# Kernel optimization log

Hardware: AMD Instinct MI355X
Metric: run time of the kernel (lower is better)

## Reference

```python
import jax, jax.numpy as jnp
import numpy as np

N = 96   # collocation points per axis
H = 64   # MLP hidden width (features[:-1])
R = 32   # CP rank (r * out_dim with out_dim=1)


def setup_inputs() -> dict:
    key = jax.random.key(0)
    ks = jax.random.split(key, 7)

    def glorot(k, shape, fan_in, fan_out):
        s = np.sqrt(2.0 / (fan_in + fan_out)).astype(np.float32)
        return jax.random.normal(k, shape, jnp.float32) * s

    return {
        "t": jax.random.uniform(ks[0], (N, 1), jnp.float32),
        "x": jax.random.uniform(ks[1], (N, 1), jnp.float32),
        "y": jax.random.uniform(ks[2], (N, 1), jnp.float32),
        "z": jax.random.uniform(ks[3], (N, 1), jnp.float32),
        "W1": glorot(ks[4], (4, 1, H), 1, H),
        "b1": jnp.zeros((4, H), jnp.float32),
        "W2": glorot(ks[5], (4, H, H), H, H),
        "b2": jnp.zeros((4, H), jnp.float32),
        "W3": glorot(ks[6], (4, H, R), H, R),
        "b3": jnp.zeros((4, R), jnp.float32),
    }


def reference(t, x, y, z, W1, b1, W2, b2, W3, b3):
    coords = (t, x, y, z)
    outs = []
    for i in range(4):  # fixed small loop over the 4 axes (distinct params)
        h = jnp.tanh(coords[i] @ W1[i] + b1[i])   # [N, H]
        h = jnp.tanh(h @ W2[i] + b2[i])           # [N, H]
        o = h @ W3[i] + b3[i]                     # [N, R]
        outs.append(o.T)                          # [R, N]
    ft, fx, fy, fz = outs
    tx = jnp.einsum('ft,fx->ftx', ft, fx)         # [R, Nt, Nx]
    txy = jnp.einsum('ftx,fy->ftxy', tx, fy)      # [R, Nt, Nx, Ny]
    pred = jnp.einsum('ftxy,fz->txyz', txy, fz)   # [Nt, Nx, Ny, Nz]
    return pred
```

## Files before the change

kernel.cpp:

```cpp
#include <hip/hip_runtime.h>

#define NPTS 96
#define HID  64
#define RANK 32

typedef float f2 __attribute__((ext_vector_type(2)));
typedef float f4 __attribute__((ext_vector_type(4)));

__global__ __launch_bounds__(64) void spinn_mlp(
    const float* __restrict__ t, const float* __restrict__ x,
    const float* __restrict__ y, const float* __restrict__ z,
    const float* __restrict__ W1, const float* __restrict__ b1,
    const float* __restrict__ W2, const float* __restrict__ b2,
    const float* __restrict__ W3, const float* __restrict__ b3,
    float* __restrict__ ws)
{
    const int n    = blockIdx.x;
    const int axis = blockIdx.y;
    const int j    = threadIdx.x;

    const float* coords[4] = { t, x, y, z };
    const float c = coords[axis][n];

    __shared__ float h1[HID];
    __shared__ float h2[HID];

    h1[j] = tanhf(fmaf(c, W1[axis * HID + j], b1[axis * HID + j]));
    __syncthreads();

    float a = b2[axis * HID + j];
    #pragma unroll
    for (int k = 0; k < HID; ++k)
        a = fmaf(h1[k], W2[(axis * HID + k) * HID + j], a);
    h2[j] = tanhf(a);
    __syncthreads();

    if (j < RANK) {
        float o = b3[axis * RANK + j];
        #pragma unroll
        for (int k = 0; k < HID; ++k)
            o = fmaf(h2[k], W3[(axis * HID + k) * RANK + j], o);
        ws[axis * RANK * NPTS + j * NPTS + n]             = o;
        ws[4 * RANK * NPTS + (axis * NPTS + n) * RANK + j] = o;
    }
}

__global__ __launch_bounds__(192) void spinn_outer(
    const float* __restrict__ ws, float* __restrict__ out)
{
    const float* plain = ws;
    const float* trans = ws + 4 * RANK * NPTS;

    const int tt  = blockIdx.x;
    const int yb  = blockIdx.y;
    const int xh  = blockIdx.z;
    const int tid = threadIdx.x;
    const int yq  = tid / 24;
    const int z4  = tid % 24;
    const int yy  = yb * 8 + yq;
    const int z0  = z4 * 4;

    const float* ftT = trans + (0 * NPTS + tt) * RANK;
    const float* fyT = trans + (2 * NPTS + yy) * RANK;
    const float* fzP = plain + 3 * RANK * NPTS;

    f2 q0[RANK], q1[RANK];
    #pragma unroll
    for (int f = 0; f < RANK; ++f) {
        const float g = ftT[f] * fyT[f];
        const float* fzf = fzP + f * NPTS + z0;
        f2 a = { fzf[0], fzf[1] };
        f2 b = { fzf[2], fzf[3] };
        q0[f] = a * g;
        q1[f] = b * g;
    }

    const float* fxT = trans + 1 * NPTS * RANK;
    const int x0 = xh * 48;
    const size_t outb = (size_t)tt * NPTS * NPTS * NPTS + (size_t)yy * NPTS + z0;

    for (int xs = 0; xs < 48; ++xs) {
        const int xx = x0 + xs;
        const float* __restrict__ fx = fxT + xx * RANK;
        f2 acc0 = { 0.f, 0.f }, acc1 = { 0.f, 0.f };
        #pragma unroll
        for (int f = 0; f < RANK; ++f) {
            const float s = fx[f];
            const f2 s2 = { s, s };
            acc0 = __builtin_elementwise_fma(s2, q0[f], acc0);
            acc1 = __builtin_elementwise_fma(s2, q1[f], acc1);
        }
        f4 res = { acc0.x, acc0.y, acc1.x, acc1.y };
        f4* dst = (f4*)(out + outb + (size_t)xx * NPTS * NPTS);
        __builtin_nontemporal_store(res, dst);
    }
}

extern "C" void kernel_launch(void* const* d_in, const int* in_sizes, int n_in,
                              void* d_out, int out_size, void* d_ws, size_t ws_size,
                              hipStream_t stream)
{
    const float* t  = (const float*)d_in[0];
    const float* x  = (const float*)d_in[1];
    const float* y  = (const float*)d_in[2];
    const float* z  = (const float*)d_in[3];
    const float* W1 = (const float*)d_in[4];
    const float* b1 = (const float*)d_in[5];
    const float* W2 = (const float*)d_in[6];
    const float* b2 = (const float*)d_in[7];
    const float* W3 = (const float*)d_in[8];
    const float* b3 = (const float*)d_in[9];

    float* ws  = (float*)d_ws;
    float* out = (float*)d_out;

    spinn_mlp<<<dim3(NPTS, 4), 64, 0, stream>>>(t, x, y, z, W1, b1, W2, b2, W3, b3, ws);

    spinn_outer<<<dim3(NPTS, 12, 2), 192, 0, stream>>>(ws, out);
}
```

Measured before the change: 90.01 us.

## Pack rank pairs into packed FMAs and defer output stores one iteration

Rewrites the outer-product inner loop to pair adjacent rank components, so each packed FMA consumes two rank terms at once. fx values are loaded as float4 vectors. Each output store is deferred to the next iteration behind a sched barrier, letting the store overlap the next row's loads and math. The change adds inline asm v_pk_fma_f32, extra accumulators and a final horizontal reduction, which changes summation order slightly and raises register pressure.

```diff
diff --git a/kernel.cpp b/kernel.cpp
--- a/kernel.cpp
+++ b/kernel.cpp
@@ -6,6 +6,8 @@
 
 typedef float f2 __attribute__((ext_vector_type(2)));
 typedef float f4 __attribute__((ext_vector_type(4)));
+
+#define TRANS_OFF (4 * RANK * NPTS)
 
 __global__ __launch_bounds__(64) void spinn_mlp(
     const float* __restrict__ t, const float* __restrict__ x,
@@ -40,17 +42,14 @@
         #pragma unroll
         for (int k = 0; k < HID; ++k)
             o = fmaf(h2[k], W3[(axis * HID + k) * RANK + j], o);
-        ws[axis * RANK * NPTS + j * NPTS + n]             = o;
-        ws[4 * RANK * NPTS + (axis * NPTS + n) * RANK + j] = o;
+        ws[axis * RANK * NPTS + j * NPTS + n]        = o;
+        ws[TRANS_OFF + (axis * NPTS + n) * RANK + j] = o;
     }
 }
 
 __global__ __launch_bounds__(192) void spinn_outer(
     const float* __restrict__ ws, float* __restrict__ out)
 {
-    const float* plain = ws;
-    const float* trans = ws + 4 * RANK * NPTS;
-
     const int tt  = blockIdx.x;
     const int yb  = blockIdx.y;
     const int xh  = blockIdx.z;
@@ -60,40 +59,80 @@
     const int yy  = yb * 8 + yq;
     const int z0  = z4 * 4;
 
-    const float* ftT = trans + (0 * NPTS + tt) * RANK;
-    const float* fyT = trans + (2 * NPTS + yy) * RANK;
-    const float* fzP = plain + 3 * RANK * NPTS;
+    const float* ftT = ws + TRANS_OFF + (0 * NPTS + tt) * RANK;
+    const float* fyT = ws + TRANS_OFF + (2 * NPTS + yy) * RANK;
+    const float* fzP = ws + 3 * RANK * NPTS;
 
-    f2 q0[RANK], q1[RANK];
+    f2 q2[16][4];
     #pragma unroll
-    for (int f = 0; f < RANK; ++f) {
-        const float g = ftT[f] * fyT[f];
-        const float* fzf = fzP + f * NPTS + z0;
-        f2 a = { fzf[0], fzf[1] };
-        f2 b = { fzf[2], fzf[3] };
-        q0[f] = a * g;
-        q1[f] = b * g;
+    for (int k = 0; k < 16; ++k) {
+        const float g0 = ftT[2 * k]     * fyT[2 * k];
+        const float g1 = ftT[2 * k + 1] * fyT[2 * k + 1];
+        #pragma unroll
+        for (int zz = 0; zz < 4; ++zz) {
+            q2[k][zz] = f2{ g0 * fzP[(2 * k) * NPTS + z0 + zz],
+                            g1 * fzP[(2 * k + 1) * NPTS + z0 + zz] };
+        }
     }
 
-    const float* fxT = trans + 1 * NPTS * RANK;
     const int x0 = xh * 48;
-    const size_t outb = (size_t)tt * NPTS * NPTS * NPTS + (size_t)yy * NPTS + z0;
+    const float* fxl = ws + TRANS_OFF + (size_t)(1 * NPTS) * RANK + (size_t)x0 * RANK;
+    asm("" : "+v"(fxl));
 
+    float* outp = out + (size_t)tt * NPTS * NPTS * NPTS
+                      + (size_t)x0 * NPTS * NPTS
+                      + (size_t)yy * NPTS + z0;
+    float* stp = outp;
+
+    f4 pend;
+
+    #pragma unroll 1
     for (int xs = 0; xs < 48; ++xs) {
-        const int xx = x0 + xs;
-        const float* __restrict__ fx = fxT + xx * RANK;
-        f2 acc0 = { 0.f, 0.f }, acc1 = { 0.f, 0.f };
+        const f4* fv = (const f4*)(fxl + (size_t)xs * RANK);
+        f4 Ld[8];
         #pragma unroll
-        for (int f = 0; f < RANK; ++f) {
-            const float s = fx[f];
-            const f2 s2 = { s, s };
-            acc0 = __builtin_elementwise_fma(s2, q0[f], acc0);
-            acc1 = __builtin_elementwise_fma(s2, q1[f], acc1);
+        for (int j = 0; j < 8; ++j) Ld[j] = fv[j];
+
+        __builtin_amdgcn_sched_barrier(0);
+
+        if (xs) {
+            __builtin_nontemporal_store(pend, (f4*)stp);
+            stp += NPTS * NPTS;
         }
-        f4 res = { acc0.x, acc0.y, acc1.x, acc1.y };
-        f4* dst = (f4*)(out + outb + (size_t)xx * NPTS * NPTS);
-        __builtin_nontemporal_store(res, dst);
+
+        f2 acc[8];
+        #pragma unroll
+        for (int c = 0; c < 8; ++c) acc[c] = f2{0.f, 0.f};
+
+        #define DO_K(Lj, lohi, kk)                                              \
+        {                                                                       \
+            f2 p_ = __builtin_shufflevector((Lj), (Lj), 2*(lohi), 2*(lohi)+1);  \
+            asm("v_pk_fma_f32 %0, %2, %3, %0\n\t"                               \
+                "v_pk_fma_f32 %1, %2, %4, %1"                                   \
+                : "+v"(acc[(((kk)&1)<<2)+0]), "+v"(acc[(((kk)&1)<<2)+1])        \
+                : "v"(p_), "v"(q2[kk][0]), "v"(q2[kk][1]));                     \
+            asm("v_pk_fma_f32 %0, %2, %3, %0\n\t"                               \
+                "v_pk_fma_f32 %1, %2, %4, %1"                                   \
+                : "+v"(acc[(((kk)&1)<<2)+2]), "+v"(acc[(((kk)&1)<<2)+3])        \
+                : "v"(p_), "v"(q2[kk][2]), "v"(q2[kk][3]));                     \
+        }
+
+        DO_K(Ld[0], 0, 0)   DO_K(Ld[0], 1, 1)
+        DO_K(Ld[1], 0, 2)   DO_K(Ld[1], 1, 3)
+        DO_K(Ld[2], 0, 4)   DO_K(Ld[2], 1, 5)
+        DO_K(Ld[3], 0, 6)   DO_K(Ld[3], 1, 7)
+        DO_K(Ld[4], 0, 8)   DO_K(Ld[4], 1, 9)
+        DO_K(Ld[5], 0, 10)  DO_K(Ld[5], 1, 11)
+        DO_K(Ld[6], 0, 12)  DO_K(Ld[6], 1, 13)
+        DO_K(Ld[7], 0, 14)  DO_K(Ld[7], 1, 15)
+        #undef DO_K
+
+        pend = f4{ (acc[0].x + acc[0].y) + (acc[4].x + acc[4].y),
+                   (acc[1].x + acc[1].y) + (acc[5].x + acc[5].y),
+                   (acc[2].x + acc[2].y) + (acc[6].x + acc[6].y),
+                   (acc[3].x + acc[3].y) + (acc[7].x + acc[7].y) };
     }
+    __builtin_nontemporal_store(pend, (f4*)stp);
 }
 
 extern "C" void kernel_launch(void* const* d_in, const int* in_sizes, int n_in,
@@ -115,6 +154,5 @@
     float* out = (float*)d_out;
 
     spinn_mlp<<<dim3(NPTS, 4), 64, 0, stream>>>(t, x, y, z, W1, b1, W2, b2, W3, b3, ws);
-
     spinn_outer<<<dim3(NPTS, 12, 2), 192, 0, stream>>>(ws, out);
 }
```

Measured after the change: 129.4 us. 43.8% more time.

## Shrink per-thread outer-product tile and pair rank terms for packed FMA

Applied to the files above, without the earlier changes.

The outer-product kernel now gives each thread 2 z-values instead of 4 and covers 24 x-slices instead of 48. The grid grows from 96x12x2 to 96x24x4 blocks, and launch bounds request 4 blocks per CU. Rank terms are paired into float2 lanes, so the fx row is read as f2 and fed straight into packed FMAs, with a horizontal add at the end. The aim is more occupancy and fewer registers per thread to better hide the store-bound output write, at the cost of narrower 8-byte stores and recomputing the q setup in more blocks.

```diff
diff --git a/kernel.cpp b/kernel.cpp
--- a/kernel.cpp
+++ b/kernel.cpp
@@ -5,7 +5,8 @@
 #define RANK 32
 
 typedef float f2 __attribute__((ext_vector_type(2)));
-typedef float f4 __attribute__((ext_vector_type(4)));
+
+#define TRANS_OFF (4 * RANK * NPTS)
 
 __global__ __launch_bounds__(64) void spinn_mlp(
     const float* __restrict__ t, const float* __restrict__ x,
@@ -40,59 +41,59 @@
         #pragma unroll
         for (int k = 0; k < HID; ++k)
             o = fmaf(h2[k], W3[(axis * HID + k) * RANK + j], o);
-        ws[axis * RANK * NPTS + j * NPTS + n]             = o;
-        ws[4 * RANK * NPTS + (axis * NPTS + n) * RANK + j] = o;
+        ws[axis * RANK * NPTS + j * NPTS + n]        = o;
+        ws[TRANS_OFF + (axis * NPTS + n) * RANK + j] = o;
     }
 }
 
-__global__ __launch_bounds__(192) void spinn_outer(
+__global__ __launch_bounds__(192, 4) void spinn_outer(
     const float* __restrict__ ws, float* __restrict__ out)
 {
-    const float* plain = ws;
-    const float* trans = ws + 4 * RANK * NPTS;
-
     const int tt  = blockIdx.x;
     const int yb  = blockIdx.y;
     const int xh  = blockIdx.z;
     const int tid = threadIdx.x;
-    const int yq  = tid / 24;
-    const int z4  = tid % 24;
-    const int yy  = yb * 8 + yq;
-    const int z0  = z4 * 4;
+    const int zp  = tid % 48;
+    const int yq  = tid / 48;
+    const int yy  = yb * 4 + yq;
+    const int z0  = zp * 2;
 
-    const float* ftT = trans + (0 * NPTS + tt) * RANK;
-    const float* fyT = trans + (2 * NPTS + yy) * RANK;
-    const float* fzP = plain + 3 * RANK * NPTS;
+    const float* ftT = ws + TRANS_OFF + (0 * NPTS + tt) * RANK;
+    const float* fyT = ws + TRANS_OFF + (2 * NPTS + yy) * RANK;
+    const float* fzP = ws + 3 * RANK * NPTS;
 
-    f2 q0[RANK], q1[RANK];
+    f2 q2[16][2];
     #pragma unroll
-    for (int f = 0; f < RANK; ++f) {
-        const float g = ftT[f] * fyT[f];
-        const float* fzf = fzP + f * NPTS + z0;
-        f2 a = { fzf[0], fzf[1] };
-        f2 b = { fzf[2], fzf[3] };
-        q0[f] = a * g;
-        q1[f] = b * g;
+    for (int k = 0; k < 16; ++k) {
+        const f2 ft2 = *(const f2*)(ftT + 2 * k);
+        const f2 fy2 = *(const f2*)(fyT + 2 * k);
+        const float g0 = ft2.x * fy2.x;
+        const float g1 = ft2.y * fy2.y;
+        const f2 za = *(const f2*)(fzP + (2 * k) * NPTS + z0);
+        const f2 zb = *(const f2*)(fzP + (2 * k + 1) * NPTS + z0);
+        q2[k][0] = f2{ g0 * za.x, g1 * zb.x };
+        q2[k][1] = f2{ g0 * za.y, g1 * zb.y };
     }
 
-    const float* fxT = trans + 1 * NPTS * RANK;
-    const int x0 = xh * 48;
-    const size_t outb = (size_t)tt * NPTS * NPTS * NPTS + (size_t)yy * NPTS + z0;
+    const int x0 = xh * 24;
+    const float* fxT = ws + TRANS_OFF + (1 * NPTS) * RANK;
+    float* outp = out + (size_t)tt * NPTS * NPTS * NPTS
+                      + (size_t)x0 * NPTS * NPTS
+                      + (size_t)yy * NPTS + z0;
 
-    for (int xs = 0; xs < 48; ++xs) {
-        const int xx = x0 + xs;
-        const float* __restrict__ fx = fxT + xx * RANK;
-        f2 acc0 = { 0.f, 0.f }, acc1 = { 0.f, 0.f };
+    #pragma unroll 2
+    for (int xs = 0; xs < 24; ++xs) {
+        const f2* fp = (const f2*)(fxT + (size_t)(x0 + xs) * RANK);
+        f2 a0 = { 0.f, 0.f }, a1 = { 0.f, 0.f };
         #pragma unroll
-        for (int f = 0; f < RANK; ++f) {
-            const float s = fx[f];
-            const f2 s2 = { s, s };
-            acc0 = __builtin_elementwise_fma(s2, q0[f], acc0);
-            acc1 = __builtin_elementwise_fma(s2, q1[f], acc1);
+        for (int k = 0; k < 16; ++k) {
+            const f2 p = fp[k];
+            a0 = __builtin_elementwise_fma(p, q2[k][0], a0);
+            a1 = __builtin_elementwise_fma(p, q2[k][1], a1);
         }
-        f4 res = { acc0.x, acc0.y, acc1.x, acc1.y };
-        f4* dst = (f4*)(out + outb + (size_t)xx * NPTS * NPTS);
-        __builtin_nontemporal_store(res, dst);
+        const f2 r = { a0.x + a0.y, a1.x + a1.y };
+        __builtin_nontemporal_store(r, (f2*)outp);
+        outp += NPTS * NPTS;
     }
 }
 
@@ -115,6 +116,5 @@
     float* out = (float*)d_out;
 
     spinn_mlp<<<dim3(NPTS, 4), 64, 0, stream>>>(t, x, y, z, W1, b1, W2, b2, W3, b3, ws);
-
-    spinn_outer<<<dim3(NPTS, 12, 2), 192, 0, stream>>>(ws, out);
+    spinn_outer<<<dim3(NPTS, 24, 4), 192, 0, stream>>>(ws, out);
 }
```

Result: faster. 85.55 us (-5.0%).

## Recast outer-product contraction as split-bf16 MFMA GEMM over (t,x)×(y,z) pairs

Applied to the files above, without the earlier changes.

The rank-32 CP contraction is rewritten as a 9216×9216 GEMM with K=32. A prep kernel forms the products ft·fx and fy·fz and stores each as hi/lo bf16 pairs, and a GEMM kernel runs three bf16 MFMAs per 16×16 tile to approximate fp32 accuracy. This moves the arithmetic onto matrix cores. In exchange it adds an extra kernel launch and workspace traffic, gives up the nontemporal stores, and loses some precision by dropping the lo×lo term. The output write of about 340MB stays the dominant cost.

```diff
diff --git a/kernel.cpp b/kernel.cpp
--- a/kernel.cpp
+++ b/kernel.cpp
@@ -1,11 +1,29 @@
 #include <hip/hip_runtime.h>
+#include <hip/hip_bf16.h>
 
 #define NPTS 96
 #define HID  64
 #define RANK 32
+#define NTX  (NPTS * NPTS)
+#define LDC  (NPTS * NPTS)
 
-typedef float f2 __attribute__((ext_vector_type(2)));
-typedef float f4 __attribute__((ext_vector_type(4)));
+#define TRANS_BYTES (4 * NPTS * RANK * 4)
+#define AHI_OFF TRANS_BYTES
+#define ALO_OFF (AHI_OFF + NTX * RANK * 2)
+#define BHI_OFF (ALO_OFF + NTX * RANK * 2)
+#define BLO_OFF (BHI_OFF + NTX * RANK * 2)
+
+typedef short s8v __attribute__((ext_vector_type(8)));
+typedef float f4v __attribute__((ext_vector_type(4)));
+
+static __device__ inline short f2bf(float f) {
+    __hip_bfloat16 h = __float2bfloat16(f);
+    return *reinterpret_cast<short*>(&h);
+}
+static __device__ inline float bf2f(short s) {
+    __hip_bfloat16 h = *reinterpret_cast<__hip_bfloat16*>(&s);
+    return __bfloat162float(h);
+}
 
 __global__ __launch_bounds__(64) void spinn_mlp(
     const float* __restrict__ t, const float* __restrict__ x,
@@ -40,59 +58,67 @@
         #pragma unroll
         for (int k = 0; k < HID; ++k)
             o = fmaf(h2[k], W3[(axis * HID + k) * RANK + j], o);
-        ws[axis * RANK * NPTS + j * NPTS + n]             = o;
-        ws[4 * RANK * NPTS + (axis * NPTS + n) * RANK + j] = o;
+        ws[(axis * NPTS + n) * RANK + j] = o;
     }
 }
 
-__global__ __launch_bounds__(192) void spinn_outer(
+__global__ __launch_bounds__(256) void spinn_prep(float* __restrict__ ws)
+{
+    const int gid = blockIdx.x * 256 + threadIdx.x;
+    const int isB = gid >= NTX;
+    const int row = isB ? gid - NTX : gid;
+    const int i0  = row / NPTS;
+    const int i1  = row % NPTS;
+
+    const float* u = ws + (((isB ? 2 : 0) * NPTS) + i0) * RANK;
+    const float* v = ws + (((isB ? 3 : 1) * NPTS) + i1) * RANK;
+    short* dhi = (short*)((char*)ws + (isB ? BHI_OFF : AHI_OFF)) + (size_t)row * RANK;
+    short* dlo = (short*)((char*)ws + (isB ? BLO_OFF : ALO_OFF)) + (size_t)row * RANK;
+
+    #pragma unroll
+    for (int k = 0; k < RANK; ++k) {
+        const float p  = u[k] * v[k];
+        const short hi = f2bf(p);
+        const short lo = f2bf(p - bf2f(hi));
+        dhi[k] = hi;
+        dlo[k] = lo;
+    }
+}
+
+__global__ __launch_bounds__(256) void spinn_gemm(
     const float* __restrict__ ws, float* __restrict__ out)
 {
-    const float* plain = ws;
-    const float* trans = ws + 4 * RANK * NPTS;
+    const short* Ahi = (const short*)((const char*)ws + AHI_OFF);
+    const short* Alo = (const short*)((const char*)ws + ALO_OFF);
+    const short* Bhi = (const short*)((const char*)ws + BHI_OFF);
+    const short* Blo = (const short*)((const char*)ws + BLO_OFF);
 
-    const int tt  = blockIdx.x;
-    const int yb  = blockIdx.y;
-    const int xh  = blockIdx.z;
-    const int tid = threadIdx.x;
-    const int yq  = tid / 24;
-    const int z4  = tid % 24;
-    const int yy  = yb * 8 + yq;
-    const int z0  = z4 * 4;
+    const int l  = threadIdx.x & 63;
+    const int w  = threadIdx.x >> 6;
+    const int I  = blockIdx.x * 4 + w;
+    const int Jb = blockIdx.y * 4;
+    const int r  = l & 15;
+    const int kb = (l >> 4) * 8;
 
-    const float* ftT = trans + (0 * NPTS + tt) * RANK;
-    const float* fyT = trans + (2 * NPTS + yy) * RANK;
-    const float* fzP = plain + 3 * RANK * NPTS;
+    const size_t arow = (size_t)(I * 16 + r) * RANK + kb;
+    const s8v ahi = *(const s8v*)(Ahi + arow);
+    const s8v alo = *(const s8v*)(Alo + arow);
 
-    f2 q0[RANK], q1[RANK];
+    float* obase = out + (size_t)(I * 16 + r) * LDC + (l >> 4) * 4;
+
     #pragma unroll
-    for (int f = 0; f < RANK; ++f) {
-        const float g = ftT[f] * fyT[f];
-        const float* fzf = fzP + f * NPTS + z0;
-        f2 a = { fzf[0], fzf[1] };
-        f2 b = { fzf[2], fzf[3] };
-        q0[f] = a * g;
-        q1[f] = b * g;
-    }
+    for (int jj = 0; jj < 4; ++jj) {
+        const int J = Jb + jj;
+        const size_t brow = (size_t)(J * 16 + r) * RANK + kb;
+        const s8v bhi = *(const s8v*)(Bhi + brow);
+        const s8v blo = *(const s8v*)(Blo + brow);
 
-    const float* fxT = trans + 1 * NPTS * RANK;
-    const int x0 = xh * 48;
-    const size_t outb = (size_t)tt * NPTS * NPTS * NPTS + (size_t)yy * NPTS + z0;
+        f4v acc = __builtin_amdgcn_mfma_f32_16x16x32_bf16(
+            bhi, ahi, (f4v){0.f, 0.f, 0.f, 0.f}, 0, 0, 0);
+        acc = __builtin_amdgcn_mfma_f32_16x16x32_bf16(bhi, alo, acc, 0, 0, 0);
+        acc = __builtin_amdgcn_mfma_f32_16x16x32_bf16(blo, ahi, acc, 0, 0, 0);
 
-    for (int xs = 0; xs < 48; ++xs) {
-        const int xx = x0 + xs;
-        const float* __restrict__ fx = fxT + xx * RANK;
-        f2 acc0 = { 0.f, 0.f }, acc1 = { 0.f, 0.f };
-        #pragma unroll
-        for (int f = 0; f < RANK; ++f) {
-            const float s = fx[f];
-            const f2 s2 = { s, s };
-            acc0 = __builtin_elementwise_fma(s2, q0[f], acc0);
-            acc1 = __builtin_elementwise_fma(s2, q1[f], acc1);
-        }
-        f4 res = { acc0.x, acc0.y, acc1.x, acc1.y };
-        f4* dst = (f4*)(out + outb + (size_t)xx * NPTS * NPTS);
-        __builtin_nontemporal_store(res, dst);
+        *(f4v*)(obase + J * 16) = acc;
     }
 }
 
@@ -115,6 +141,6 @@
     float* out = (float*)d_out;
 
     spinn_mlp<<<dim3(NPTS, 4), 64, 0, stream>>>(t, x, y, z, W1, b1, W2, b2, W3, b3, ws);
-
-    spinn_outer<<<dim3(NPTS, 12, 2), 192, 0, stream>>>(ws, out);
+    spinn_prep<<<(2 * NTX) / 256, 256, 0, stream>>>(ws);
+    spinn_gemm<<<dim3(NTX / 16 / 4, NTX / 16 / 4), 256, 0, stream>>>(ws, out);
 }
```

Result: slower. 97.80 us (+8.7%).
